# Kernel tuning notes

Measured on AMD Instinct MI355X. Metric: run time of the kernel, lower is better.

The kernel has to match this reference:

```python
import jax, jax.numpy as jnp
import numpy as np
import math

HIDDEN = 256
NUM_GAUSSIANS = 64
NUM_FILTERS = 256
CUTOFF = 1.0
COSINE_OFFSET = 0.0
N_NODES = 10000
N_EDGES = 320000


def ssp(x):
    # shifted softplus: softplus(x) - log(2)
    return jax.nn.softplus(x) - jnp.log(2.0).astype(x.dtype)


def setup_inputs() -> dict:
    key = jax.random.key(0)
    ks = jax.random.split(key, 12)

    def xavier(k, fan_out, fan_in):
        a = math.sqrt(6.0 / (fan_in + fan_out))
        return jax.random.uniform(k, (fan_out, fan_in), jnp.float32, -a, a)

    x = jax.random.normal(ks[0], (N_NODES, HIDDEN), jnp.float32)
    ji_pairs = jax.random.randint(ks[1], (2, N_EDGES), 0, N_NODES, jnp.int64)
    e_ji = jax.random.uniform(ks[2], (N_EDGES,), jnp.float32)  # distances in [0, cutoff)
    e_ji_basis = jax.random.normal(ks[3], (N_EDGES, NUM_GAUSSIANS), jnp.float32)

    return {
        "x": x,
        "ji_pairs": ji_pairs,
        "e_ji": e_ji,
        "e_ji_basis": e_ji_basis,
        # filter_nn: Linear(G->F), ssp, Linear(F->F)
        "fw1": xavier(ks[4], NUM_FILTERS, NUM_GAUSSIANS),
        "fb1": jnp.zeros((NUM_FILTERS,), jnp.float32),
        "fw2": xavier(ks[5], NUM_FILTERS, NUM_FILTERS),
        "fb2": jnp.zeros((NUM_FILTERS,), jnp.float32),
        # CFConv linears
        "w1": xavier(ks[6], NUM_FILTERS, HIDDEN),            # linear1, no bias
        "w2": xavier(ks[7], HIDDEN, NUM_FILTERS),            # linear2
        "b2": jnp.zeros((HIDDEN,), jnp.float32),
        # linear3
        "w3": xavier(ks[8], HIDDEN, HIDDEN),
        "b3": jnp.zeros((HIDDEN,), jnp.float32),
    }


def reference(x, ji_pairs, e_ji, e_ji_basis, fw1, fb1, fw2, fb2, w1, w2, b2, w3, b3):
    pi = jnp.asarray(math.pi, x.dtype)
    # cosine cutoff: C = 0.25 * (cos((e - off) * pi / (cutoff - off)) + 1)
    C = 0.25 * (jnp.cos((e_ji - COSINE_OFFSET) * pi / (CUTOFF - COSINE_OFFSET)) + 1.0)
    # filter network on edge RBF features: [E, F]
    W = ssp(e_ji_basis @ fw1.T + fb1) @ fw2.T + fb2
    W = W * C[:, None]
    # linear1 (no bias): [N, F]
    h = x @ w1.T
    # message: x_j * W, gathered from source nodes ji_pairs[0]
    src, dst = ji_pairs[0], ji_pairs[1]
    msg = h[src] * W                                   # [E, F]
    agg = jax.ops.segment_sum(msg, dst, num_segments=x.shape[0])  # [N, F]
    # linear2
    out = agg @ w2.T + b2
    # interaction block tail: act + linear3
    out = ssp(out) @ w3.T + b3
    return out
```

## Files before the change

kernel.cpp:

```cpp
#include <hip/hip_runtime.h>
#include <hip/hip_bf16.h>

typedef __bf16 bf16_t;
typedef float f32x4 __attribute__((ext_vector_type(4)));
typedef __bf16 bf16x8 __attribute__((ext_vector_type(8)));

#define NNODES 10000
#define NEDGES 320000
#define NPAD   10048
#define NB2    (NEDGES / 64)
#define GSLOT  5

#define OFF_AGG   256
#define OFF_JIN   (OFF_AGG  + (size_t)NPAD * 256 * 4)
#define OFF_HIST  (OFF_JIN  + (size_t)2 * NEDGES * 4)
#define OFF_CUR   (OFF_HIST + 10240 * 4)
#define OFF_CSR   (OFF_CUR  + 10240 * 4)
#define OFF_PERM  (OFF_CSR  + 10240 * 4)
#define OFF_SRCS  (OFF_PERM + (size_t)NEDGES * 4)
#define OFF_DSTS  (OFF_SRCS + (size_t)NEDGES * 4)
#define OFF_CES   (OFF_DSTS + (size_t)NEDGES * 4)
#define OFF_CE    (OFF_CES  + (size_t)NEDGES * 4)
#define OFF_WB    (OFF_CE   + (size_t)NEDGES * 4)
#define FW1B 0
#define FW2B 16384
#define W1B  81920
#define W2B  147456
#define W3B  212992
#define FB1B 278528
#define FB2B 278784
#define B2B  279040
#define B3B  279296
#define WBN  279552
#define WS_NEED (OFF_WB + (size_t)WBN * 2)

__device__ __forceinline__ float ssp_f(float v) {
    return fmaxf(v, 0.f) + __logf(1.f + __expf(-fabsf(v))) - 0.69314718055994531f;
}
__device__ __forceinline__ f32x4 mfma16(bf16x8 a, bf16x8 b, f32x4 c) {
    return __builtin_amdgcn_mfma_f32_16x16x32_bf16(a, b, c, 0, 0, 0);
}
template<bool ISB>
__device__ __forceinline__ bf16x8 ld8(const void* p, size_t off) {
    if constexpr (ISB) return *(const bf16x8*)((const bf16_t*)p + off);
    else {
        const float* f = (const float*)p + off;
        f32x4 lo = *(const f32x4*)f, hi = *(const f32x4*)(f + 4);
        bf16x8 r;
        for (int j = 0; j < 4; ++j) { r[j] = (bf16_t)lo[j]; r[j + 4] = (bf16_t)hi[j]; }
        return r;
    }
}
template<bool ISB>
__device__ __forceinline__ void st1(void* p, size_t off, float v) {
    if constexpr (ISB) ((bf16_t*)p)[off] = (bf16_t)v;
    else               ((float*)p)[off] = v;
}
__device__ __forceinline__ float ld1r(bool isb, const void* p, size_t off) {
    return isb ? (float)((const bf16_t*)p)[off] : ((const float*)p)[off];
}

__global__ __launch_bounds__(256) void detect_kernel(
    const void* __restrict__ x, const int* __restrict__ jraw,
    int* __restrict__ flags, int* __restrict__ hist)
{
    __shared__ int cnt, hi;
    if (threadIdx.x == 0) { cnt = 0; hi = 0; }
    __syncthreads();
    const unsigned short* xw = (const unsigned short*)x;
    int local = 0;
    for (int i = threadIdx.x; i < 2048; i += 256) {
        unsigned int e = (xw[2 * i] >> 7) & 0xFF;
        if (e >= 100 && e <= 141) local++;
    }
    atomicAdd(&cnt, local);
    int v = 0;
    for (int i = threadIdx.x; i < 1024; i += 256) v |= jraw[2 * i + 1];
    if (v != 0) atomicOr(&hi, 1);
    for (int i = threadIdx.x; i < 10240; i += 256) hist[i] = 0;
    __syncthreads();
    if (threadIdx.x == 0) { flags[0] = (cnt > 1024) ? 1 : 0; flags[1] = (hi == 0) ? 1 : 0; }
}

__global__ __launch_bounds__(256) void prep_kernel(
    const int* __restrict__ raw, const int* __restrict__ flags,
    const void* __restrict__ e_ji,
    const void* fw1, const void* fb1, const void* fw2, const void* fb2,
    const void* w1, const void* w2, const void* b2, const void* w3, const void* b3,
    int* __restrict__ jin, int* __restrict__ hist, float* __restrict__ ce,
    bf16_t* __restrict__ wb, float* __restrict__ agg)
{
    const bool is64 = (flags[1] != 0);
    const bool isb  = (flags[0] != 0);
    const int gid = blockIdx.x * 256 + threadIdx.x;
    if (gid < 2 * NEDGES) {
        int iv = is64 ? raw[2 * gid] : raw[gid];
        iv = iv < 0 ? 0 : (iv >= NNODES ? NNODES - 1 : iv);
        jin[gid] = iv;
        if (gid >= NEDGES) atomicAdd(&hist[iv], 1);
    }
    if (gid < NEDGES)
        ce[gid] = 0.25f * (cosf(3.14159265358979f * ld1r(isb, e_ji, gid)) + 1.0f);
    if (gid < WBN) {
        int g = gid; const void* s; int so;
        if      (g < FW2B) { s = fw1; so = g - FW1B; }
        else if (g < W1B)  { s = fw2; so = g - FW2B; }
        else if (g < W2B)  { s = w1;  so = g - W1B; }
        else if (g < W3B)  { s = w2;  so = g - W2B; }
        else if (g < FB1B) { s = w3;  so = g - W3B; }
        else if (g < FB2B) { s = fb1; so = g - FB1B; }
        else if (g < B2B)  { s = fb2; so = g - FB2B; }
        else if (g < B3B)  { s = b2;  so = g - B2B; }
        else               { s = b3;  so = g - B3B; }
        wb[gid] = (bf16_t)ld1r(isb, s, so);
    }
    f32x4 z = {0.f, 0.f, 0.f, 0.f};
    for (int i = gid; i < NPAD * 256 / 4; i += 2500 * 256)
        ((f32x4*)agg)[i] = z;
}

__global__ __launch_bounds__(256) void scan_kernel(
    const int* __restrict__ hist, int* __restrict__ cur, int* __restrict__ csr)
{
    __shared__ int s[256];
    const int t = threadIdx.x;
    int loc[40]; int sum = 0;
    const int base = t * 40;
    for (int j = 0; j < 40; ++j) {
        int i = base + j;
        loc[j] = (i < NNODES) ? hist[i] : 0;
        sum += loc[j];
    }
    s[t] = sum; __syncthreads();
    for (int off = 1; off < 256; off <<= 1) {
        int v = (t >= off) ? s[t - off] : 0;
        __syncthreads();
        if (t >= off) s[t] += v;
        __syncthreads();
    }
    int pre = (t == 0) ? 0 : s[t - 1];
    for (int j = 0; j < 40; ++j) {
        int i = base + j;
        cur[i] = pre;
        csr[i] = pre;
        pre += loc[j];
    }
}

__global__ __launch_bounds__(256) void scatter_kernel(
    const int* __restrict__ jin, const float* __restrict__ ce,
    int* __restrict__ cur, int* __restrict__ perm,
    int* __restrict__ src_s, int* __restrict__ dst_s, float* __restrict__ ce_s)
{
    int e = blockIdx.x * 256 + threadIdx.x;
    if (e < NEDGES) {
        int d = jin[NEDGES + e];
        int pos = atomicAdd(&cur[d], 1);
        perm[pos]  = e;
        src_s[pos] = jin[e];
        dst_s[pos] = d;
        ce_s[pos]  = ce[e];
    }
}

template<bool ISB>
__global__ __launch_bounds__(256, 2) void h_gemm_kernel(
    const void* __restrict__ x, const bf16_t* __restrict__ wb,
    bf16_t* __restrict__ h, const int* __restrict__ flags)
{
    if ((flags[0] != 0) != ISB) return;
    const bf16_t* w1b = wb + W1B;
    const int w = threadIdx.x >> 6, L = threadIdx.x & 63;
    const int lane16 = L & 15, quad = L >> 4;
    const int nb = blockIdx.x * 64, cb = w * 64;
    f32x4 acc[4][4] = {};
    for (int kc = 0; kc < 8; ++kc) {
        const int ko = kc * 32 + quad * 8;
        bf16x8 af[4], bfr[4];
        for (int mt = 0; mt < 4; ++mt) {
            int row = nb + mt * 16 + lane16;
            if (row >= NNODES) row = NNODES - 1;
            af[mt] = ld8<ISB>(x, (size_t)row * 256 + ko);
        }
        for (int nt = 0; nt < 4; ++nt)
            bfr[nt] = *(const bf16x8*)(w1b + (size_t)(cb + nt * 16 + lane16) * 256 + ko);
        for (int mt = 0; mt < 4; ++mt)
            for (int nt = 0; nt < 4; ++nt)
                acc[mt][nt] = mfma16(af[mt], bfr[nt], acc[mt][nt]);
    }
    for (int mt = 0; mt < 4; ++mt)
        for (int r = 0; r < 4; ++r) {
            int row = nb + mt * 16 + quad * 4 + r;
            if (row < NNODES)
                for (int nt = 0; nt < 4; ++nt)
                    h[(size_t)row * 256 + cb + nt * 16 + lane16] = (bf16_t)acc[mt][nt][r];
        }
}

template<bool ISB>
__global__ __launch_bounds__(256, 4) void edge_kernel_sp(
    const void* __restrict__ basis, const int* __restrict__ perm,
    const int* __restrict__ src_s, const int* __restrict__ dst_s,
    const float* __restrict__ ce_s,
    const bf16_t* __restrict__ wb, const bf16_t* __restrict__ h,
    float* __restrict__ agg, const int* __restrict__ flags)
{
    if ((flags[0] != 0) != ISB) return;
    __shared__ bf16_t T[64][264];
    __shared__ float G[GSLOT][260];
    __shared__ int sperm[64], ssrc[64], sdst[64];
    __shared__ float sce[64];
    const int tid = threadIdx.x;
    const int w = tid >> 6, L = tid & 63;
    const int lane16 = L & 15, quad = L >> 4;
    const int cb = w * 64;
    const int bid = (int)blockIdx.x;
    const int e0 = ((bid & 7) * (NB2 / 8) + (bid >> 3)) * 64;

    if      (w == 0) sperm[L] = perm[e0 + L];
    else if (w == 1) ssrc[L] = src_s[e0 + L];
    else if (w == 2) sdst[L] = dst_s[e0 + L];
    else             sce[L]  = ce_s[e0 + L];
    for (int i = tid; i < GSLOT * 260; i += 256) (&G[0][0])[i] = 0.f;

    const bf16_t* fw1b = wb + FW1B;
    const bf16_t* fw2b = wb + FW2B;
    float fb1v[4], fb2v[4];
    for (int nt = 0; nt < 4; ++nt) {
        fb1v[nt] = (float)wb[FB1B + cb + nt * 16 + lane16];
        fb2v[nt] = (float)wb[FB2B + cb + nt * 16 + lane16];
    }
    __syncthreads();

    const int sbase = sdst[0];
    const int span  = sdst[63] - sbase + 1;
    const bool fbk  = (span > GSLOT);

    const int hrow = tid >> 2, hseg = tid & 3;
    bf16x8 hreg[8];
    {
        const bf16_t* hs = h + (size_t)ssrc[hrow] * 256 + hseg * 64;
        #pragma unroll
        for (int j = 0; j < 8; ++j) hreg[j] = ((const bf16x8*)hs)[j];
    }

    int prow[4];
    for (int mt = 0; mt < 4; ++mt) prow[mt] = sperm[mt * 16 + lane16];

    f32x4 acc1[4][4] = {};
    for (int kc = 0; kc < 2; ++kc) {
        const int ko = kc * 32 + quad * 8;
        bf16x8 af[4], bfr[4];
        for (int mt = 0; mt < 4; ++mt)
            af[mt] = ld8<ISB>(basis, (size_t)prow[mt] * 64 + ko);
        for (int nt = 0; nt < 4; ++nt)
            bfr[nt] = *(const bf16x8*)(fw1b + (size_t)(cb + nt * 16 + lane16) * 64 + ko);
        for (int mt = 0; mt < 4; ++mt)
            for (int nt = 0; nt < 4; ++nt)
                acc1[mt][nt] = mfma16(af[mt], bfr[nt], acc1[mt][nt]);
    }
    for (int nt = 0; nt < 4; ++nt) {
        int col = cb + nt * 16 + lane16;
        for (int mt = 0; mt < 4; ++mt)
            for (int r = 0; r < 4; ++r)
                T[mt * 16 + quad * 4 + r][col] = (bf16_t)ssp_f(acc1[mt][nt][r] + fb1v[nt]);
    }
    __syncthreads();

    f32x4 acc2[4][4] = {};
    for (int kc = 0; kc < 8; ++kc) {
        const int ko = kc * 32 + quad * 8;
        bf16x8 af[4], bfr[4];
        for (int mt = 0; mt < 4; ++mt)
            af[mt] = *(const bf16x8*)(&T[mt * 16 + lane16][ko]);
        for (int nt = 0; nt < 4; ++nt)
            bfr[nt] = *(const bf16x8*)(fw2b + (size_t)(cb + nt * 16 + lane16) * 256 + ko);
        for (int mt = 0; mt < 4; ++mt)
            for (int nt = 0; nt < 4; ++nt)
                acc2[mt][nt] = mfma16(af[mt], bfr[nt], acc2[mt][nt]);
    }
    __syncthreads();

    {
        bf16_t* dp = &T[hrow][hseg * 64];
        #pragma unroll
        for (int j = 0; j < 8; ++j) ((bf16x8*)dp)[j] = hreg[j];
    }
    __syncthreads();

    float run[4] = {0, 0, 0, 0};
    int curn = -1;
    for (int mt = 0; mt < 4; ++mt)
        for (int r = 0; r < 4; ++r) {
            int row = mt * 16 + quad * 4 + r;
            int n = sdst[row];
            if (n != curn) {
                if (curn >= 0) {
                    if (!fbk)
                        for (int nt = 0; nt < 4; ++nt)
                            atomicAdd(&G[curn - sbase][cb + nt * 16 + lane16], run[nt]);
                    else
                        for (int nt = 0; nt < 4; ++nt)
                            atomicAdd(&agg[(size_t)curn * 256 + cb + nt * 16 + lane16], run[nt]);
                }
                curn = n;
                run[0] = run[1] = run[2] = run[3] = 0.f;
            }
            float cv = sce[row];
            for (int nt = 0; nt < 4; ++nt) {
                int col = cb + nt * 16 + lane16;
                run[nt] += (acc2[mt][nt][r] + fb2v[nt]) * cv * (float)T[row][col];
            }
        }
    if (curn >= 0) {
        if (!fbk)
            for (int nt = 0; nt < 4; ++nt)
                atomicAdd(&G[curn - sbase][cb + nt * 16 + lane16], run[nt]);
        else
            for (int nt = 0; nt < 4; ++nt)
                atomicAdd(&agg[(size_t)curn * 256 + cb + nt * 16 + lane16], run[nt]);
    }
    __syncthreads();

    if (!fbk) {
        for (int s = 0; s < span; ++s)
            atomicAdd(&agg[(size_t)(sbase + s) * 256 + tid], G[s][tid]);
    }
}

template<bool ISB>
__global__ __launch_bounds__(256, 2) void out_kernel(
    const float* __restrict__ agg, const bf16_t* __restrict__ wb,
    void* __restrict__ out, const int* __restrict__ flags)
{
    if ((flags[0] != 0) != ISB) return;
    const bf16_t* w2b = wb + W2B;
    const bf16_t* w3b = wb + W3B;
    __shared__ bf16_t U[64][264];
    const int w = threadIdx.x >> 6, L = threadIdx.x & 63;
    const int lane16 = L & 15, quad = L >> 4;
    const int nb = blockIdx.x * 64, cb = w * 64;

    f32x4 acc[4][4] = {};
    for (int kc = 0; kc < 8; ++kc) {
        const int ko = kc * 32 + quad * 8;
        bf16x8 af[4], bfr[4];
        for (int mt = 0; mt < 4; ++mt) {
            int row = nb + mt * 16 + lane16;
            const float* p = agg + (size_t)row * 256 + ko;
            f32x4 lo = *(const f32x4*)p, hi = *(const f32x4*)(p + 4);
            bf16x8 a;
            for (int j = 0; j < 4; ++j) { a[j] = (bf16_t)lo[j]; a[j + 4] = (bf16_t)hi[j]; }
            af[mt] = a;
        }
        for (int nt = 0; nt < 4; ++nt)
            bfr[nt] = *(const bf16x8*)(w2b + (size_t)(cb + nt * 16 + lane16) * 256 + ko);
        for (int mt = 0; mt < 4; ++mt)
            for (int nt = 0; nt < 4; ++nt)
                acc[mt][nt] = mfma16(af[mt], bfr[nt], acc[mt][nt]);
    }
    for (int nt = 0; nt < 4; ++nt) {
        int col = cb + nt * 16 + lane16;
        float bias = (float)wb[B2B + col];
        for (int mt = 0; mt < 4; ++mt)
            for (int r = 0; r < 4; ++r)
                U[mt * 16 + quad * 4 + r][col] = (bf16_t)ssp_f(acc[mt][nt][r] + bias);
    }
    __syncthreads();

    f32x4 acc2[4][4] = {};
    for (int kc = 0; kc < 8; ++kc) {
        const int ko = kc * 32 + quad * 8;
        bf16x8 af[4], bfr[4];
        for (int mt = 0; mt < 4; ++mt)
            af[mt] = *(const bf16x8*)(&U[mt * 16 + lane16][ko]);
        for (int nt = 0; nt < 4; ++nt)
            bfr[nt] = *(const bf16x8*)(w3b + (size_t)(cb + nt * 16 + lane16) * 256 + ko);
        for (int mt = 0; mt < 4; ++mt)
            for (int nt = 0; nt < 4; ++nt)
                acc2[mt][nt] = mfma16(af[mt], bfr[nt], acc2[mt][nt]);
    }
    for (int mt = 0; mt < 4; ++mt)
        for (int r = 0; r < 4; ++r) {
            int row = nb + mt * 16 + quad * 4 + r;
            if (row < NNODES)
                for (int nt = 0; nt < 4; ++nt) {
                    int col = cb + nt * 16 + lane16;
                    st1<ISB>(out, (size_t)row * 256 + col,
                             acc2[mt][nt][r] + (float)wb[B3B + col]);
                }
        }
}

extern "C" void kernel_launch(void* const* d_in, const int* in_sizes, int n_in,
                              void* d_out, int out_size, void* d_ws, size_t ws_size,
                              hipStream_t stream) {
    const void* x     = d_in[0];
    const int*  ji    = (const int*)d_in[1];
    const void* e_ji  = d_in[2];
    const void* basis = d_in[3];
    const void* fw1   = d_in[4];
    const void* fb1   = d_in[5];
    const void* fw2   = d_in[6];
    const void* fb2   = d_in[7];
    const void* w1    = d_in[8];
    const void* w2    = d_in[9];
    const void* b2    = d_in[10];
    const void* w3    = d_in[11];
    const void* b3    = d_in[12];

    if (ws_size < WS_NEED) return;

    char* W = (char*)d_ws;
    int*    flags = (int*)W;
    float*  agg   = (float*)(W + OFF_AGG);
    int*    jin   = (int*)(W + OFF_JIN);
    int*    hist  = (int*)(W + OFF_HIST);
    int*    cur   = (int*)(W + OFF_CUR);
    int*    csr   = (int*)(W + OFF_CSR);
    int*    perm  = (int*)(W + OFF_PERM);
    int*    src_s = (int*)(W + OFF_SRCS);
    int*    dst_s = (int*)(W + OFF_DSTS);
    float*  ce_s  = (float*)(W + OFF_CES);
    float*  ce    = (float*)(W + OFF_CE);
    bf16_t* wb    = (bf16_t*)(W + OFF_WB);
    bf16_t* h     = (bf16_t*)d_out;

    detect_kernel<<<1, 256, 0, stream>>>(x, ji, flags, hist);
    prep_kernel<<<2500, 256, 0, stream>>>(ji, flags, e_ji, fw1, fb1, fw2, fb2,
                                          w1, w2, b2, w3, b3, jin, hist, ce, wb, agg);
    scan_kernel<<<1, 256, 0, stream>>>(hist, cur, csr);
    scatter_kernel<<<1250, 256, 0, stream>>>(jin, ce, cur, perm, src_s, dst_s, ce_s);
    h_gemm_kernel<true ><<<157, 256, 0, stream>>>(x, wb, h, flags);
    h_gemm_kernel<false><<<157, 256, 0, stream>>>(x, wb, h, flags);
    edge_kernel_sp<true ><<<NB2, 256, 0, stream>>>(basis, perm, src_s, dst_s, ce_s, wb, h, agg, flags);
    edge_kernel_sp<false><<<NB2, 256, 0, stream>>>(basis, perm, src_s, dst_s, ce_s, wb, h, agg, flags);
    out_kernel<true ><<<157, 256, 0, stream>>>(agg, wb, d_out, flags);
    out_kernel<false><<<157, 256, 0, stream>>>(agg, wb, d_out, flags);
}
```

Baseline: 515.9 us.

## Pre-permute basis into bf16 sorted order during scatter for contiguous edge loads

The scatter kernel now also writes each edge's 64-wide basis row, converted to bf16, into a workspace buffer at its destination-sorted position. A new edge kernel reads this contiguous bf16 buffer straight into registers at the start, instead of gathering rows through the permutation (and converting fp32 on the fly). It also drops one of the two ISB-templated launches. The cost is an extra write and read of a 41 MB buffer, plus a workspace-size check that falls back to the old path when the workspace is too small.

```diff
diff --git a/kernel.cpp b/kernel.cpp
--- a/kernel.cpp
+++ b/kernel.cpp
@@ -33,6 +33,8 @@
 #define B3B  279296
 #define WBN  279552
 #define WS_NEED (OFF_WB + (size_t)WBN * 2)
+#define OFF_BASC  ((WS_NEED + 255) & ~(size_t)255)
+#define WS_NEED_BIG (OFF_BASC + (size_t)(NEDGES + 64) * 64 * 2)
 
 __device__ __forceinline__ float ssp_f(float v) {
     return fmaxf(v, 0.f) + __logf(1.f + __expf(-fabsf(v))) - 0.69314718055994531f;
@@ -50,6 +52,14 @@
         for (int j = 0; j < 4; ++j) { r[j] = (bf16_t)lo[j]; r[j + 4] = (bf16_t)hi[j]; }
         return r;
     }
+}
+__device__ __forceinline__ bf16x8 ld8r(bool isb, const void* p, size_t off) {
+    if (isb) return *(const bf16x8*)((const bf16_t*)p + off);
+    const float* f = (const float*)p + off;
+    f32x4 lo = *(const f32x4*)f, hi = *(const f32x4*)(f + 4);
+    bf16x8 r;
+    for (int j = 0; j < 4; ++j) { r[j] = (bf16_t)lo[j]; r[j + 4] = (bf16_t)hi[j]; }
+    return r;
 }
 template<bool ISB>
 __device__ __forceinline__ void st1(void* p, size_t off, float v) {
@@ -149,17 +159,25 @@
 
 __global__ __launch_bounds__(256) void scatter_kernel(
     const int* __restrict__ jin, const float* __restrict__ ce,
+    const void* __restrict__ basis, const int* __restrict__ flags,
     int* __restrict__ cur, int* __restrict__ perm,
-    int* __restrict__ src_s, int* __restrict__ dst_s, float* __restrict__ ce_s)
+    int* __restrict__ src_s, int* __restrict__ dst_s, float* __restrict__ ce_s,
+    bf16_t* __restrict__ basc, int doconv)
 {
     int e = blockIdx.x * 256 + threadIdx.x;
-    if (e < NEDGES) {
-        int d = jin[NEDGES + e];
-        int pos = atomicAdd(&cur[d], 1);
-        perm[pos]  = e;
-        src_s[pos] = jin[e];
-        dst_s[pos] = d;
-        ce_s[pos]  = ce[e];
+    if (e >= NEDGES) return;
+    int d = jin[NEDGES + e];
+    int pos = atomicAdd(&cur[d], 1);
+    perm[pos]  = e;
+    src_s[pos] = jin[e];
+    dst_s[pos] = d;
+    ce_s[pos]  = ce[e];
+    if (doconv) {
+        const bool isb = (flags[0] != 0);
+        bf16_t* dp = basc + (size_t)pos * 64;
+        #pragma unroll
+        for (int j = 0; j < 8; ++j)
+            *(bf16x8*)(dp + j * 8) = ld8r(isb, basis, (size_t)e * 64 + j * 8);
     }
 }
 
@@ -197,18 +215,16 @@
         }
 }
 
-template<bool ISB>
-__global__ __launch_bounds__(256, 4) void edge_kernel_sp(
-    const void* __restrict__ basis, const int* __restrict__ perm,
+__global__ __launch_bounds__(256, 4) void edge_fast_sp(
+    const bf16_t* __restrict__ basc,
     const int* __restrict__ src_s, const int* __restrict__ dst_s,
     const float* __restrict__ ce_s,
     const bf16_t* __restrict__ wb, const bf16_t* __restrict__ h,
-    float* __restrict__ agg, const int* __restrict__ flags)
-{
-    if ((flags[0] != 0) != ISB) return;
+    float* __restrict__ agg)
+{
     __shared__ bf16_t T[64][264];
     __shared__ float G[GSLOT][260];
-    __shared__ int sperm[64], ssrc[64], sdst[64];
+    __shared__ int ssrc[64], sdst[64];
     __shared__ float sce[64];
     const int tid = threadIdx.x;
     const int w = tid >> 6, L = tid & 63;
@@ -217,10 +233,17 @@
     const int bid = (int)blockIdx.x;
     const int e0 = ((bid & 7) * (NB2 / 8) + (bid >> 3)) * 64;
 
-    if      (w == 0) sperm[L] = perm[e0 + L];
-    else if (w == 1) ssrc[L] = src_s[e0 + L];
-    else if (w == 2) sdst[L] = dst_s[e0 + L];
-    else             sce[L]  = ce_s[e0 + L];
+    bf16x8 breg[2][4];
+    #pragma unroll
+    for (int kc = 0; kc < 2; ++kc)
+        #pragma unroll
+        for (int mt = 0; mt < 4; ++mt)
+            breg[kc][mt] = *(const bf16x8*)(basc +
+                (size_t)(e0 + mt * 16 + lane16) * 64 + kc * 32 + quad * 8);
+
+    if      (w == 0) ssrc[L] = src_s[e0 + L];
+    else if (w == 1) sdst[L] = dst_s[e0 + L];
+    else if (w == 2) sce[L]  = ce_s[e0 + L];
     for (int i = tid; i < GSLOT * 260; i += 256) (&G[0][0])[i] = 0.f;
 
     const bf16_t* fw1b = wb + FW1B;
@@ -244,20 +267,16 @@
         for (int j = 0; j < 8; ++j) hreg[j] = ((const bf16x8*)hs)[j];
     }
 
-    int prow[4];
-    for (int mt = 0; mt < 4; ++mt) prow[mt] = sperm[mt * 16 + lane16];
-
     f32x4 acc1[4][4] = {};
+    #pragma unroll
     for (int kc = 0; kc < 2; ++kc) {
         const int ko = kc * 32 + quad * 8;
-        bf16x8 af[4], bfr[4];
-        for (int mt = 0; mt < 4; ++mt)
-            af[mt] = ld8<ISB>(basis, (size_t)prow[mt] * 64 + ko);
+        bf16x8 bfr[4];
         for (int nt = 0; nt < 4; ++nt)
             bfr[nt] = *(const bf16x8*)(fw1b + (size_t)(cb + nt * 16 + lane16) * 64 + ko);
         for (int mt = 0; mt < 4; ++mt)
             for (int nt = 0; nt < 4; ++nt)
-                acc1[mt][nt] = mfma16(af[mt], bfr[nt], acc1[mt][nt]);
+                acc1[mt][nt] = mfma16(breg[kc][mt], bfr[nt], acc1[mt][nt]);
     }
     for (int nt = 0; nt < 4; ++nt) {
         int col = cb + nt * 16 + lane16;
@@ -329,6 +348,137 @@
 }
 
 template<bool ISB>
+__global__ __launch_bounds__(256, 4) void edge_kernel_sp(
+    const void* __restrict__ basis, const int* __restrict__ perm,
+    const int* __restrict__ src_s, const int* __restrict__ dst_s,
+    const float* __restrict__ ce_s,
+    const bf16_t* __restrict__ wb, const bf16_t* __restrict__ h,
+    float* __restrict__ agg, const int* __restrict__ flags)
+{
+    if ((flags[0] != 0) != ISB) return;
+    __shared__ bf16_t T[64][264];
+    __shared__ float G[GSLOT][260];
+    __shared__ int sperm[64], ssrc[64], sdst[64];
+    __shared__ float sce[64];
+    const int tid = threadIdx.x;
+    const int w = tid >> 6, L = tid & 63;
+    const int lane16 = L & 15, quad = L >> 4;
+    const int cb = w * 64;
+    const int bid = (int)blockIdx.x;
+    const int e0 = ((bid & 7) * (NB2 / 8) + (bid >> 3)) * 64;
+
+    if      (w == 0) sperm[L] = perm[e0 + L];
+    else if (w == 1) ssrc[L] = src_s[e0 + L];
+    else if (w == 2) sdst[L] = dst_s[e0 + L];
+    else             sce[L]  = ce_s[e0 + L];
+    for (int i = tid; i < GSLOT * 260; i += 256) (&G[0][0])[i] = 0.f;
+
+    const bf16_t* fw1b = wb + FW1B;
+    const bf16_t* fw2b = wb + FW2B;
+    float fb1v[4], fb2v[4];
+    for (int nt = 0; nt < 4; ++nt) {
+        fb1v[nt] = (float)wb[FB1B + cb + nt * 16 + lane16];
+        fb2v[nt] = (float)wb[FB2B + cb + nt * 16 + lane16];
+    }
+    __syncthreads();
+
+    const int sbase = sdst[0];
+    const int span  = sdst[63] - sbase + 1;
+    const bool fbk  = (span > GSLOT);
+
+    const int hrow = tid >> 2, hseg = tid & 3;
+    bf16x8 hreg[8];
+    {
+        const bf16_t* hs = h + (size_t)ssrc[hrow] * 256 + hseg * 64;
+        #pragma unroll
+        for (int j = 0; j < 8; ++j) hreg[j] = ((const bf16x8*)hs)[j];
+    }
+
+    int prow[4];
+    for (int mt = 0; mt < 4; ++mt) prow[mt] = sperm[mt * 16 + lane16];
+
+    f32x4 acc1[4][4] = {};
+    for (int kc = 0; kc < 2; ++kc) {
+        const int ko = kc * 32 + quad * 8;
+        bf16x8 af[4], bfr[4];
+        for (int mt = 0; mt < 4; ++mt)
+            af[mt] = ld8<ISB>(basis, (size_t)prow[mt] * 64 + ko);
+        for (int nt = 0; nt < 4; ++nt)
+            bfr[nt] = *(const bf16x8*)(fw1b + (size_t)(cb + nt * 16 + lane16) * 64 + ko);
+        for (int mt = 0; mt < 4; ++mt)
+            for (int nt = 0; nt < 4; ++nt)
+                acc1[mt][nt] = mfma16(af[mt], bfr[nt], acc1[mt][nt]);
+    }
+    for (int nt = 0; nt < 4; ++nt) {
+        int col = cb + nt * 16 + lane16;
+        for (int mt = 0; mt < 4; ++mt)
+            for (int r = 0; r < 4; ++r)
+                T[mt * 16 + quad * 4 + r][col] = (bf16_t)ssp_f(acc1[mt][nt][r] + fb1v[nt]);
+    }
+    __syncthreads();
+
+    f32x4 acc2[4][4] = {};
+    for (int kc = 0; kc < 8; ++kc) {
+        const int ko = kc * 32 + quad * 8;
+        bf16x8 af[4], bfr[4];
+        for (int mt = 0; mt < 4; ++mt)
+            af[mt] = *(const bf16x8*)(&T[mt * 16 + lane16][ko]);
+        for (int nt = 0; nt < 4; ++nt)
+            bfr[nt] = *(const bf16x8*)(fw2b + (size_t)(cb + nt * 16 + lane16) * 256 + ko);
+        for (int mt = 0; mt < 4; ++mt)
+            for (int nt = 0; nt < 4; ++nt)
+                acc2[mt][nt] = mfma16(af[mt], bfr[nt], acc2[mt][nt]);
+    }
+    __syncthreads();
+
+    {
+        bf16_t* dp = &T[hrow][hseg * 64];
+        #pragma unroll
+        for (int j = 0; j < 8; ++j) ((bf16x8*)dp)[j] = hreg[j];
+    }
+    __syncthreads();
+
+    float run[4] = {0, 0, 0, 0};
+    int curn = -1;
+    for (int mt = 0; mt < 4; ++mt)
+        for (int r = 0; r < 4; ++r) {
+            int row = mt * 16 + quad * 4 + r;
+            int n = sdst[row];
+            if (n != curn) {
+                if (curn >= 0) {
+                    if (!fbk)
+                        for (int nt = 0; nt < 4; ++nt)
+                            atomicAdd(&G[curn - sbase][cb + nt * 16 + lane16], run[nt]);
+                    else
+                        for (int nt = 0; nt < 4; ++nt)
+                            atomicAdd(&agg[(size_t)curn * 256 + cb + nt * 16 + lane16], run[nt]);
+                }
+                curn = n;
+                run[0] = run[1] = run[2] = run[3] = 0.f;
+            }
+            float cv = sce[row];
+            for (int nt = 0; nt < 4; ++nt) {
+                int col = cb + nt * 16 + lane16;
+                run[nt] += (acc2[mt][nt][r] + fb2v[nt]) * cv * (float)T[row][col];
+            }
+        }
+    if (curn >= 0) {
+        if (!fbk)
+            for (int nt = 0; nt < 4; ++nt)
+                atomicAdd(&G[curn - sbase][cb + nt * 16 + lane16], run[nt]);
+        else
+            for (int nt = 0; nt < 4; ++nt)
+                atomicAdd(&agg[(size_t)curn * 256 + cb + nt * 16 + lane16], run[nt]);
+    }
+    __syncthreads();
+
+    if (!fbk) {
+        for (int s = 0; s < span; ++s)
+            atomicAdd(&agg[(size_t)(sbase + s) * 256 + tid], G[s][tid]);
+    }
+}
+
+template<bool ISB>
 __global__ __launch_bounds__(256, 2) void out_kernel(
     const float* __restrict__ agg, const bf16_t* __restrict__ wb,
     void* __restrict__ out, const int* __restrict__ flags)
@@ -410,6 +560,7 @@
     const void* b3    = d_in[12];
 
     if (ws_size < WS_NEED) return;
+    const bool bigws = ws_size >= WS_NEED_BIG;
 
     char* W = (char*)d_ws;
     int*    flags = (int*)W;
@@ -424,17 +575,23 @@
     float*  ce_s  = (float*)(W + OFF_CES);
     float*  ce    = (float*)(W + OFF_CE);
     bf16_t* wb    = (bf16_t*)(W + OFF_WB);
+    bf16_t* basc  = (bf16_t*)(W + OFF_BASC);
     bf16_t* h     = (bf16_t*)d_out;
 
     detect_kernel<<<1, 256, 0, stream>>>(x, ji, flags, hist);
     prep_kernel<<<2500, 256, 0, stream>>>(ji, flags, e_ji, fw1, fb1, fw2, fb2,
                                           w1, w2, b2, w3, b3, jin, hist, ce, wb, agg);
     scan_kernel<<<1, 256, 0, stream>>>(hist, cur, csr);
-    scatter_kernel<<<1250, 256, 0, stream>>>(jin, ce, cur, perm, src_s, dst_s, ce_s);
+    scatter_kernel<<<1250, 256, 0, stream>>>(jin, ce, basis, flags, cur, perm,
+                                             src_s, dst_s, ce_s, basc, bigws ? 1 : 0);
     h_gemm_kernel<true ><<<157, 256, 0, stream>>>(x, wb, h, flags);
     h_gemm_kernel<false><<<157, 256, 0, stream>>>(x, wb, h, flags);
-    edge_kernel_sp<true ><<<NB2, 256, 0, stream>>>(basis, perm, src_s, dst_s, ce_s, wb, h, agg, flags);
-    edge_kernel_sp<false><<<NB2, 256, 0, stream>>>(basis, perm, src_s, dst_s, ce_s, wb, h, agg, flags);
+    if (bigws) {
+        edge_fast_sp<<<NB2, 256, 0, stream>>>(basc, src_s, dst_s, ce_s, wb, h, agg);
+    } else {
+        edge_kernel_sp<true ><<<NB2, 256, 0, stream>>>(basis, perm, src_s, dst_s, ce_s, wb, h, agg, flags);
+        edge_kernel_sp<false><<<NB2, 256, 0, stream>>>(basis, perm, src_s, dst_s, ce_s, wb, h, agg, flags);
+    }
     out_kernel<true ><<<157, 256, 0, stream>>>(agg, wb, d_out, flags);
     out_kernel<false><<<157, 256, 0, stream>>>(agg, wb, d_out, flags);
 }
```

Result: slower. 534.0 us (+3.5%).
